# Optimization experiments

Hardware: AMD Instinct MI355X
Metric: run time of the kernel (lower is better)

Reference implementation:

```python
import jax, jax.numpy as jnp
import numpy as np

B, T, N, F_IN, F_OUT, E = 4, 12, 2048, 64, 64, 32768


def setup_inputs() -> dict:
    key = jax.random.key(0)
    ks = jax.random.split(key, 10)
    s = 1.0 / np.sqrt(F_IN)
    return {
        "x": jax.random.normal(ks[0], (B, T, N, F_IN), dtype=jnp.float32),
        "edge_index": jax.random.randint(ks[1], (2, E), 0, N, dtype=jnp.int64),
        "Wk": jax.random.normal(ks[2], (F_IN, F_OUT), dtype=jnp.float32) * s,
        "bk": jax.random.normal(ks[3], (F_OUT,), dtype=jnp.float32) * s,
        "Wq": jax.random.normal(ks[4], (F_IN, F_OUT), dtype=jnp.float32) * s,
        "bq": jax.random.normal(ks[5], (F_OUT,), dtype=jnp.float32) * s,
        "Wv": jax.random.normal(ks[6], (F_IN, F_OUT), dtype=jnp.float32) * s,
        "bv": jax.random.normal(ks[7], (F_OUT,), dtype=jnp.float32) * s,
        "Wskip": jax.random.normal(ks[8], (F_IN, F_OUT), dtype=jnp.float32) * s,
        "bias": jax.random.normal(ks[9], (F_OUT,), dtype=jnp.float32) * s,
    }


def reference(x, edge_index, Wk, bk, Wq, bq, Wv, bv, Wskip, bias):
    b, t, n, _ = x.shape
    xs = x.reshape(b * t, n, -1)                       # (b t) n f
    # per-node projections (small GEMMs)
    k = xs @ Wk + bk                                   # key from target nodes
    q = xs @ Wq + bq                                   # query from source nodes
    v = xs @ Wv + bv                                   # value from source nodes
    src, dst = edge_index[0], edge_index[1]            # j -> i (source_to_target)
    # per-edge gate + message: LeakyReLU(k_i + q_j) * v_j  [(b t), E, f_out]
    msg = jax.nn.leaky_relu(k[:, dst] + q[:, src], negative_slope=0.01) * v[:, src]
    # scatter-add aggregation at target nodes
    agg = jnp.zeros_like(k).at[:, dst].add(msg)
    out = agg + xs @ Wskip + bias
    return out.reshape(b, t, n, -1)
```

## Files before the change

### kernel.cpp

```cpp
#include <hip/hip_runtime.h>

#define BT 48
#define NN 2048
#define FF 64
#define EE 32768
#define ROWS (BT*NN)
#define PRB 256

typedef __attribute__((ext_vector_type(2))) _Float16 half2v;
typedef __attribute__((ext_vector_type(8))) _Float16 half8v;
typedef __attribute__((ext_vector_type(4))) float float4v;

__device__ __forceinline__ unsigned cvt2h(float lo, float hi){
    union { half2v h; unsigned u; } c;
    c.h = half2v{(_Float16)lo, (_Float16)hi};
    return c.u;
}
__device__ __forceinline__ half2v h2(unsigned u){
    union { unsigned u; half2v h; } c; c.u = u; return c.h;
}

__global__ __launch_bounds__(256) void proj_kernel(
    const float* __restrict__ x,
    const float* __restrict__ Wk, const float* __restrict__ bk,
    const float* __restrict__ Wq, const float* __restrict__ bq,
    const float* __restrict__ Wv, const float* __restrict__ bv,
    const float* __restrict__ Ws, const float* __restrict__ bs,
    unsigned* __restrict__ Kh, unsigned* __restrict__ QV,
    float* __restrict__ out, int* __restrict__ meta)
{
    if (blockIdx.x == 0 && threadIdx.x < 8) meta[threadIdx.x] = 0;

    const int tid = threadIdx.x;
    const int w  = tid >> 6;
    const int l  = tid & 63;
    const int lr = l & 15;
    const int lh = l >> 4;
    const float* Wm = (w==0)?Wk:(w==1)?Wq:(w==2)?Wv:Ws;
    const float* bm = (w==0)?bk:(w==1)?bq:(w==2)?bv:bs;

    union FragH { unsigned u[4]; half8v h; };

    FragH af[4][2];
    #pragma unroll
    for (int ft=0;ft<4;ft++)
        #pragma unroll
        for (int h=0;h<2;h++)
            #pragma unroll
            for (int jj=0;jj<4;jj++){
                const int k0 = h*32 + lh*8 + 2*jj;
                af[ft][h].u[jj] = cvt2h(Wm[(size_t)k0*FF + ft*16 + lr],
                                        Wm[(size_t)(k0+1)*FF + ft*16 + lr]);
            }

    float4 bias4[4];
    #pragma unroll
    for (int ft=0;ft<4;ft++) bias4[ft] = *(const float4*)(bm + ft*16 + lh*4);

    const int row0 = blockIdx.x * PRB;
    #pragma unroll 4
    for (int rt=0; rt<PRB/16; ++rt){
        const float* xr = x + (size_t)(row0 + rt*16 + lr)*FF + lh*8;
        const float4 xa0 = *(const float4*)(xr);
        const float4 xa1 = *(const float4*)(xr + 4);
        const float4 xb0 = *(const float4*)(xr + 32);
        const float4 xb1 = *(const float4*)(xr + 36);
        FragH b0, b1;
        b0.u[0]=cvt2h(xa0.x,xa0.y); b0.u[1]=cvt2h(xa0.z,xa0.w);
        b0.u[2]=cvt2h(xa1.x,xa1.y); b0.u[3]=cvt2h(xa1.z,xa1.w);
        b1.u[0]=cvt2h(xb0.x,xb0.y); b1.u[1]=cvt2h(xb0.z,xb0.w);
        b1.u[2]=cvt2h(xb1.x,xb1.y); b1.u[3]=cvt2h(xb1.z,xb1.w);

        const size_t row = (size_t)(row0 + rt*16 + lr);
        #pragma unroll
        for (int ft=0;ft<4;ft++){
            float4v acc = float4v{bias4[ft].x, bias4[ft].y, bias4[ft].z, bias4[ft].w};
            acc = __builtin_amdgcn_mfma_f32_16x16x32_f16(af[ft][0].h, b0.h, acc, 0,0,0);
            acc = __builtin_amdgcn_mfma_f32_16x16x32_f16(af[ft][1].h, b1.h, acc, 0,0,0);
            const int p0 = ft*8 + lh*2;
            if (w == 0){
                uint2 st; st.x = cvt2h(acc[0],acc[1]); st.y = cvt2h(acc[2],acc[3]);
                *(uint2*)(Kh + row*32 + p0) = st;
            } else if (w == 1){
                QV[row*FF + 2*p0]     = cvt2h(acc[0],acc[1]);
                QV[row*FF + 2*(p0+1)] = cvt2h(acc[2],acc[3]);
            } else if (w == 2){
                QV[row*FF + 2*p0 + 1]     = cvt2h(acc[0],acc[1]);
                QV[row*FF + 2*(p0+1) + 1] = cvt2h(acc[2],acc[3]);
            } else {
                *(float4*)(out + row*FF + ft*16 + lh*4) =
                    make_float4(acc[0],acc[1],acc[2],acc[3]);
            }
        }
    }
}

__device__ __forceinline__ void gbar(int* ctr, int nblk){
    __syncthreads();
    if (threadIdx.x == 0){
        __threadfence();
        atomicAdd(ctr, 1);
        while (__hip_atomic_load(ctr, __ATOMIC_ACQUIRE, __HIP_MEMORY_SCOPE_AGENT) < nblk) {}
    }
    __syncthreads();
}

__global__ __launch_bounds__(256) void csr_kernel(
    const unsigned int* __restrict__ ew,
    int* __restrict__ flag, int* __restrict__ bar,
    int* __restrict__ deg, int* __restrict__ offs,
    int* __restrict__ cur, int* __restrict__ elist)
{
    const int t = threadIdx.x, b = blockIdx.x;
    const int gtid = b*256 + t;

    for (int i=gtid; i<NN; i+=16384) deg[i] = 0;
    if (gtid < 16) elist[EE + gtid] = 0;
    unsigned f = 0;
    for (int i=gtid; i<8192; i+=16384) f |= ew[2*i+1];
    if (f) atomicOr((unsigned int*)flag, f);
    gbar(bar+0, 64);
    const bool i64 = (*flag == 0);

    for (int e=gtid; e<EE; e+=16384){
        const int d = i64 ? (int)ew[2*(EE+e)] : (int)ew[EE+e];
        atomicAdd(&deg[d], 1);
    }
    gbar(bar+1, 64);

    if (b == 0){
        __shared__ int wsums[4];
        const int base = t*8;
        int v[8], pre[8];
        #pragma unroll
        for (int j=0;j<8;j++) v[j] = deg[base+j];
        pre[0] = 0;
        #pragma unroll
        for (int j=1;j<8;j++) pre[j] = pre[j-1] + v[j-1];
        const int s = pre[7] + v[7];
        int inc = s;
        const int lane = t & 63, wid = t >> 6;
        #pragma unroll
        for (int d=1; d<64; d<<=1){ int tt = __shfl_up(inc, d, 64); if (lane>=d) inc += tt; }
        if (lane == 63) wsums[wid] = inc;
        __syncthreads();
        if (t == 0){ int a=0; for (int k2=0;k2<4;k2++){ int tt=wsums[k2]; wsums[k2]=a; a+=tt; } }
        __syncthreads();
        const int excl = wsums[wid] + (inc - s);
        #pragma unroll
        for (int j=0;j<8;j++){ offs[base+j] = excl + pre[j]; cur[base+j] = excl + pre[j]; }
        if (t == 255) offs[NN] = excl + s;
    }
    gbar(bar+2, 64);

    for (int e=gtid; e<EE; e+=16384){
        int d, s;
        if (i64){ d = (int)ew[2*(EE+e)]; s = (int)ew[2*e]; }
        else    { d = (int)ew[EE+e];     s = (int)ew[e];   }
        const int pos = atomicAdd(&cur[d], 1);
        elist[pos] = s;
    }
}

#define HEDGE(U) { \
    half2v g01 = k01 + h2((U).x); \
    g01 = __builtin_elementwise_max(g01, g01*c001); \
    acc01 += g01 * h2((U).y); \
    half2v g23 = k23 + h2((U).z); \
    g23 = __builtin_elementwise_max(g23, g23*c001); \
    acc23 += g23 * h2((U).w); }
#define HEDGEM(U, M) { \
    half2v g01 = k01 + h2((U).x); \
    g01 = __builtin_elementwise_max(g01, g01*c001); \
    acc01 += g01 * (h2((U).y) * (M)); \
    half2v g23 = k23 + h2((U).z); \
    g23 = __builtin_elementwise_max(g23, g23*c001); \
    acc23 += g23 * (h2((U).w) * (M)); }

__global__ __launch_bounds__(256) void agg_kernel(
    const unsigned* __restrict__ Kh, const unsigned* __restrict__ QV,
    const int* __restrict__ offs, const int* __restrict__ elist,
    float* __restrict__ out)
{
    const int tid  = threadIdx.x;
    const int lane = tid & 63;
    const int w    = tid >> 6;
    const int b    = blockIdx.x;
    const int xcd  = b & 7;
    const int li   = b >> 3;
    const int bt   = xcd*6 + (li >> 9);
    const int node = ((li & 511) << 2) | w;
    const int sub  = lane >> 4;
    const int fq   = lane & 15;
    const size_t S = (size_t)NN*FF;

    const uint2 ku = *(const uint2*)(Kh + ((size_t)bt*NN + node)*32 + 2*fq);
    const half2v k01 = h2(ku.x), k23 = h2(ku.y);
    const half2v c001 = half2v{(_Float16)0.01f, (_Float16)0.01f};
    const half2v one2 = half2v{(_Float16)1.f, (_Float16)1.f};
    const half2v zero2 = half2v{(_Float16)0.f, (_Float16)0.f};
    const unsigned* QVb = QV + (size_t)bt*S;

    half2v acc01 = zero2, acc23 = zero2;
    const int s0 = offs[node], s1 = offs[node+1];

    for (int i = s0; i < s1; i += 16){
        const int rem  = s1 - i;
        const int4 ev = *(const int4*)(elist + i + 4*sub);
        const uint4 u0 = *(const uint4*)(QVb + (((unsigned)ev.x)<<6) + (fq<<2));
        const uint4 u1 = *(const uint4*)(QVb + (((unsigned)ev.y)<<6) + (fq<<2));
        const uint4 u2 = *(const uint4*)(QVb + (((unsigned)ev.z)<<6) + (fq<<2));
        const uint4 u3 = *(const uint4*)(QVb + (((unsigned)ev.w)<<6) + (fq<<2));
        if (rem >= 16){
            HEDGE(u0); HEDGE(u1); HEDGE(u2); HEDGE(u3);
        } else {
            const half2v m0 = (4*sub+0 < rem) ? one2 : zero2;
            const half2v m1 = (4*sub+1 < rem) ? one2 : zero2;
            const half2v m2 = (4*sub+2 < rem) ? one2 : zero2;
            const half2v m3 = (4*sub+3 < rem) ? one2 : zero2;
            HEDGEM(u0, m0); HEDGEM(u1, m1); HEDGEM(u2, m2); HEDGEM(u3, m3);
        }
    }

    float4 acc = make_float4((float)acc01[0], (float)acc01[1],
                             (float)acc23[0], (float)acc23[1]);

    acc.x += __shfl_xor(acc.x, 16, 64); acc.y += __shfl_xor(acc.y, 16, 64);
    acc.z += __shfl_xor(acc.z, 16, 64); acc.w += __shfl_xor(acc.w, 16, 64);
    acc.x += __shfl_xor(acc.x, 32, 64); acc.y += __shfl_xor(acc.y, 32, 64);
    acc.z += __shfl_xor(acc.z, 32, 64); acc.w += __shfl_xor(acc.w, 32, 64);

    if (sub == 0){
        const size_t rowb = ((size_t)bt*NN + node)*FF;
        const float4 sk = *(const float4*)(out + rowb + fq*4);
        float4 r;
        r.x = acc.x + sk.x; r.y = acc.y + sk.y;
        r.z = acc.z + sk.z; r.w = acc.w + sk.w;
        *(float4*)(out + rowb + fq*4) = r;
    }
}

extern "C" void kernel_launch(void* const* d_in, const int* in_sizes, int n_in,
                              void* d_out, int out_size, void* d_ws, size_t ws_size,
                              hipStream_t stream)
{
    const float* x  = (const float*)d_in[0];
    const unsigned int* ew = (const unsigned int*)d_in[1];
    const float* Wk = (const float*)d_in[2];
    const float* bk = (const float*)d_in[3];
    const float* Wq = (const float*)d_in[4];
    const float* bq = (const float*)d_in[5];
    const float* Wv = (const float*)d_in[6];
    const float* bv = (const float*)d_in[7];
    const float* Ws = (const float*)d_in[8];
    const float* bs = (const float*)d_in[9];
    float* out = (float*)d_out;

    const size_t n = (size_t)ROWS*FF;
    unsigned* Kh = (unsigned*)d_ws;
    unsigned* QV = Kh + (size_t)ROWS*32;
    int* meta  = (int*)(QV + n);
    int* flag  = meta;
    int* bar   = meta + 4;
    int* deg   = meta + 16;
    int* offs  = deg + NN;
    int* cur   = offs + NN + 16;
    int* elist = cur + NN;

    hipLaunchKernelGGL(proj_kernel, dim3(ROWS/PRB), dim3(256), 0, stream,
                       x, Wk,bk, Wq,bq, Wv,bv, Ws,bs, Kh, QV, out, meta);
    hipLaunchKernelGGL(csr_kernel, dim3(64), dim3(256), 0, stream,
                       ew, flag, bar, deg, offs, cur, elist);
    hipLaunchKernelGGL(agg_kernel, dim3(ROWS/4), dim3(256), 0, stream,
                       Kh, QV, offs, elist, out);
}
```

Baseline: 103.5 us.

## Prepack weights, pair projections per wave, and aggregate two timesteps per node

Adds a one-block kernel that converts the four weight matrices once into packed half-precision MFMA fragment layout, so projection blocks load fragments directly instead of converting them per block. The projection kernel now gives each wave two matrices (K+skip or Q+V), which lets Q and V be stored together as one 16-byte write, and uses smaller row tiles across more blocks. The aggregation kernel now handles two batch-timesteps per node in each wave, reusing the edge-list loads and CSR offsets across both and issuing twice as many independent gathers per iteration. This trades an extra kernel launch and higher register pressure for less redundant weight conversion, fewer edge-index reads and more memory-level parallelism.

```diff
diff --git a/kernel.cpp b/kernel.cpp
--- a/kernel.cpp
+++ b/kernel.cpp
@@ -5,7 +5,6 @@
 #define FF 64
 #define EE 32768
 #define ROWS (BT*NN)
-#define PRB 256
 
 typedef __attribute__((ext_vector_type(2))) _Float16 half2v;
 typedef __attribute__((ext_vector_type(8))) _Float16 half8v;
@@ -20,47 +19,67 @@
     union { unsigned u; half2v h; } c; c.u = u; return c.h;
 }
 
+union FragH { unsigned u[4]; half8v h; uint4 u4; };
+
+__global__ __launch_bounds__(256) void wpack_kernel(
+    const float* __restrict__ Wk, const float* __restrict__ Wq,
+    const float* __restrict__ Wv, const float* __restrict__ Ws,
+    unsigned* __restrict__ Wp, int* __restrict__ meta)
+{
+    const int t = threadIdx.x;
+    if (t < 8) meta[t] = 0;
+    for (int idx = t; idx < 8192; idx += 256){
+        const int mat = idx >> 11;
+        const int r   = idx & 2047;
+        const int ft  = r >> 9;
+        const int h   = (r >> 8) & 1;
+        const int l   = (r >> 2) & 63;
+        const int jj  = r & 3;
+        const float* W = (mat==0)?Wk:(mat==1)?Wq:(mat==2)?Wv:Ws;
+        const int k0 = h*32 + (l>>4)*8 + 2*jj;
+        const int c  = ft*16 + (l&15);
+        Wp[idx] = cvt2h(W[(size_t)k0*FF + c], W[(size_t)(k0+1)*FF + c]);
+    }
+}
+
 __global__ __launch_bounds__(256) void proj_kernel(
-    const float* __restrict__ x,
-    const float* __restrict__ Wk, const float* __restrict__ bk,
-    const float* __restrict__ Wq, const float* __restrict__ bq,
-    const float* __restrict__ Wv, const float* __restrict__ bv,
-    const float* __restrict__ Ws, const float* __restrict__ bs,
+    const float* __restrict__ x, const unsigned* __restrict__ Wp,
+    const float* __restrict__ bk, const float* __restrict__ bq,
+    const float* __restrict__ bv, const float* __restrict__ bs,
     unsigned* __restrict__ Kh, unsigned* __restrict__ QV,
-    float* __restrict__ out, int* __restrict__ meta)
-{
-    if (blockIdx.x == 0 && threadIdx.x < 8) meta[threadIdx.x] = 0;
-
+    float* __restrict__ out)
+{
     const int tid = threadIdx.x;
     const int w  = tid >> 6;
     const int l  = tid & 63;
     const int lr = l & 15;
     const int lh = l >> 4;
-    const float* Wm = (w==0)?Wk:(w==1)?Wq:(w==2)?Wv:Ws;
-    const float* bm = (w==0)?bk:(w==1)?bq:(w==2)?bv:bs;
-
-    union FragH { unsigned u[4]; half8v h; };
-
-    FragH af[4][2];
+    const int wm = w & 1;
+    const int matA = wm ? 1 : 0;
+    const int matB = wm ? 2 : 3;
+    const float* bmA = wm ? bq : bk;
+    const float* bmB = wm ? bv : bs;
+
+    FragH afA[4][2], afB[4][2];
     #pragma unroll
     for (int ft=0;ft<4;ft++)
         #pragma unroll
-        for (int h=0;h<2;h++)
-            #pragma unroll
-            for (int jj=0;jj<4;jj++){
-                const int k0 = h*32 + lh*8 + 2*jj;
-                af[ft][h].u[jj] = cvt2h(Wm[(size_t)k0*FF + ft*16 + lr],
-                                        Wm[(size_t)(k0+1)*FF + ft*16 + lr]);
-            }
-
-    float4 bias4[4];
+        for (int h=0;h<2;h++){
+            afA[ft][h].u4 = *(const uint4*)(Wp + ((matA*4+ft)*2+h)*256 + l*4);
+            afB[ft][h].u4 = *(const uint4*)(Wp + ((matB*4+ft)*2+h)*256 + l*4);
+        }
+    float4 biasA[4], biasB[4];
     #pragma unroll
-    for (int ft=0;ft<4;ft++) bias4[ft] = *(const float4*)(bm + ft*16 + lh*4);
-
-    const int row0 = blockIdx.x * PRB;
-    #pragma unroll 4
-    for (int rt=0; rt<PRB/16; ++rt){
-        const float* xr = x + (size_t)(row0 + rt*16 + lr)*FF + lh*8;
+    for (int ft=0;ft<4;ft++){
+        biasA[ft] = *(const float4*)(bmA + ft*16 + lh*4);
+        biasB[ft] = *(const float4*)(bmB + ft*16 + lh*4);
+    }
+
+    const int row0 = blockIdx.x * 128 + (w>>1)*64;
+    #pragma unroll 2
+    for (int rt=0; rt<4; ++rt){
+        const int r16 = row0 + rt*16;
+        const float* xr = x + (size_t)(r16 + lr)*FF + lh*8;
         const float4 xa0 = *(const float4*)(xr);
         const float4 xa1 = *(const float4*)(xr + 4);
         const float4 xb0 = *(const float4*)(xr + 32);
@@ -71,25 +90,25 @@
         b1.u[0]=cvt2h(xb0.x,xb0.y); b1.u[1]=cvt2h(xb0.z,xb0.w);
         b1.u[2]=cvt2h(xb1.x,xb1.y); b1.u[3]=cvt2h(xb1.z,xb1.w);
 
-        const size_t row = (size_t)(row0 + rt*16 + lr);
+        const size_t row = (size_t)(r16 + lr);
         #pragma unroll
         for (int ft=0;ft<4;ft++){
-            float4v acc = float4v{bias4[ft].x, bias4[ft].y, bias4[ft].z, bias4[ft].w};
-            acc = __builtin_amdgcn_mfma_f32_16x16x32_f16(af[ft][0].h, b0.h, acc, 0,0,0);
-            acc = __builtin_amdgcn_mfma_f32_16x16x32_f16(af[ft][1].h, b1.h, acc, 0,0,0);
-            const int p0 = ft*8 + lh*2;
-            if (w == 0){
-                uint2 st; st.x = cvt2h(acc[0],acc[1]); st.y = cvt2h(acc[2],acc[3]);
-                *(uint2*)(Kh + row*32 + p0) = st;
-            } else if (w == 1){
-                QV[row*FF + 2*p0]     = cvt2h(acc[0],acc[1]);
-                QV[row*FF + 2*(p0+1)] = cvt2h(acc[2],acc[3]);
-            } else if (w == 2){
-                QV[row*FF + 2*p0 + 1]     = cvt2h(acc[0],acc[1]);
-                QV[row*FF + 2*(p0+1) + 1] = cvt2h(acc[2],acc[3]);
+            float4v aA = float4v{biasA[ft].x, biasA[ft].y, biasA[ft].z, biasA[ft].w};
+            aA = __builtin_amdgcn_mfma_f32_16x16x32_f16(afA[ft][0].h, b0.h, aA, 0,0,0);
+            aA = __builtin_amdgcn_mfma_f32_16x16x32_f16(afA[ft][1].h, b1.h, aA, 0,0,0);
+            float4v aB = float4v{biasB[ft].x, biasB[ft].y, biasB[ft].z, biasB[ft].w};
+            aB = __builtin_amdgcn_mfma_f32_16x16x32_f16(afB[ft][0].h, b0.h, aB, 0,0,0);
+            aB = __builtin_amdgcn_mfma_f32_16x16x32_f16(afB[ft][1].h, b1.h, aB, 0,0,0);
+            if (wm == 0){
+                uint2 st; st.x = cvt2h(aA[0],aA[1]); st.y = cvt2h(aA[2],aA[3]);
+                *(uint2*)(Kh + row*32 + ft*8 + lh*2) = st;
+                *(float4*)(out + row*FF + ft*16 + lh*4) =
+                    make_float4(aB[0],aB[1],aB[2],aB[3]);
             } else {
-                *(float4*)(out + row*FF + ft*16 + lh*4) =
-                    make_float4(acc[0],acc[1],acc[2],acc[3]);
+                uint4 st;
+                st.x = cvt2h(aA[0],aA[1]); st.y = cvt2h(aB[0],aB[1]);
+                st.z = cvt2h(aA[2],aA[3]); st.w = cvt2h(aB[2],aB[3]);
+                *(uint4*)(QV + row*FF + ft*16 + lh*4) = st;
             }
         }
     }
@@ -162,20 +181,20 @@
     }
 }
 
-#define HEDGE(U) { \
-    half2v g01 = k01 + h2((U).x); \
+#define HEDGE2(U, KA, KB, A01, A23) { \
+    half2v g01 = (KA) + h2((U).x); \
     g01 = __builtin_elementwise_max(g01, g01*c001); \
-    acc01 += g01 * h2((U).y); \
-    half2v g23 = k23 + h2((U).z); \
+    (A01) += g01 * h2((U).y); \
+    half2v g23 = (KB) + h2((U).z); \
     g23 = __builtin_elementwise_max(g23, g23*c001); \
-    acc23 += g23 * h2((U).w); }
-#define HEDGEM(U, M) { \
-    half2v g01 = k01 + h2((U).x); \
+    (A23) += g23 * h2((U).w); }
+#define HEDGE2M(U, KA, KB, A01, A23, M) { \
+    half2v g01 = (KA) + h2((U).x); \
     g01 = __builtin_elementwise_max(g01, g01*c001); \
-    acc01 += g01 * (h2((U).y) * (M)); \
-    half2v g23 = k23 + h2((U).z); \
+    (A01) += g01 * (h2((U).y) * (M)); \
+    half2v g23 = (KB) + h2((U).z); \
     g23 = __builtin_elementwise_max(g23, g23*c001); \
-    acc23 += g23 * (h2((U).w) * (M)); }
+    (A23) += g23 * (h2((U).w) * (M)); }
 
 __global__ __launch_bounds__(256) void agg_kernel(
     const unsigned* __restrict__ Kh, const unsigned* __restrict__ QV,
@@ -188,55 +207,82 @@
     const int b    = blockIdx.x;
     const int xcd  = b & 7;
     const int li   = b >> 3;
-    const int bt   = xcd*6 + (li >> 9);
+    const int pr   = xcd*3 + (li >> 9);
     const int node = ((li & 511) << 2) | w;
     const int sub  = lane >> 4;
     const int fq   = lane & 15;
+    const int bt0  = pr*2;
     const size_t S = (size_t)NN*FF;
 
-    const uint2 ku = *(const uint2*)(Kh + ((size_t)bt*NN + node)*32 + 2*fq);
-    const half2v k01 = h2(ku.x), k23 = h2(ku.y);
+    const uint2 ku0 = *(const uint2*)(Kh + ((size_t)bt0*NN + node)*32 + 2*fq);
+    const uint2 ku1 = *(const uint2*)(Kh + ((size_t)(bt0+1)*NN + node)*32 + 2*fq);
+    const half2v k01a = h2(ku0.x), k23a = h2(ku0.y);
+    const half2v k01b = h2(ku1.x), k23b = h2(ku1.y);
     const half2v c001 = half2v{(_Float16)0.01f, (_Float16)0.01f};
     const half2v one2 = half2v{(_Float16)1.f, (_Float16)1.f};
     const half2v zero2 = half2v{(_Float16)0.f, (_Float16)0.f};
-    const unsigned* QVb = QV + (size_t)bt*S;
-
-    half2v acc01 = zero2, acc23 = zero2;
+    const unsigned* QV0 = QV + (size_t)bt0*S;
+    const unsigned* QV1 = QV0 + S;
+
+    half2v a01_0 = zero2, a23_0 = zero2;
+    half2v a01_1 = zero2, a23_1 = zero2;
     const int s0 = offs[node], s1 = offs[node+1];
 
     for (int i = s0; i < s1; i += 16){
         const int rem  = s1 - i;
         const int4 ev = *(const int4*)(elist + i + 4*sub);
-        const uint4 u0 = *(const uint4*)(QVb + (((unsigned)ev.x)<<6) + (fq<<2));
-        const uint4 u1 = *(const uint4*)(QVb + (((unsigned)ev.y)<<6) + (fq<<2));
-        const uint4 u2 = *(const uint4*)(QVb + (((unsigned)ev.z)<<6) + (fq<<2));
-        const uint4 u3 = *(const uint4*)(QVb + (((unsigned)ev.w)<<6) + (fq<<2));
+        const unsigned o0 = (((unsigned)ev.x)<<6) + (fq<<2);
+        const unsigned o1 = (((unsigned)ev.y)<<6) + (fq<<2);
+        const unsigned o2 = (((unsigned)ev.z)<<6) + (fq<<2);
+        const unsigned o3 = (((unsigned)ev.w)<<6) + (fq<<2);
+        const uint4 u00 = *(const uint4*)(QV0 + o0);
+        const uint4 u10 = *(const uint4*)(QV1 + o0);
+        const uint4 u01 = *(const uint4*)(QV0 + o1);
+        const uint4 u11 = *(const uint4*)(QV1 + o1);
+        const uint4 u02 = *(const uint4*)(QV0 + o2);
+        const uint4 u12 = *(const uint4*)(QV1 + o2);
+        const uint4 u03 = *(const uint4*)(QV0 + o3);
+        const uint4 u13 = *(const uint4*)(QV1 + o3);
         if (rem >= 16){
-            HEDGE(u0); HEDGE(u1); HEDGE(u2); HEDGE(u3);
+            HEDGE2(u00, k01a, k23a, a01_0, a23_0); HEDGE2(u10, k01b, k23b, a01_1, a23_1);
+            HEDGE2(u01, k01a, k23a, a01_0, a23_0); HEDGE2(u11, k01b, k23b, a01_1, a23_1);
+            HEDGE2(u02, k01a, k23a, a01_0, a23_0); HEDGE2(u12, k01b, k23b, a01_1, a23_1);
+            HEDGE2(u03, k01a, k23a, a01_0, a23_0); HEDGE2(u13, k01b, k23b, a01_1, a23_1);
         } else {
             const half2v m0 = (4*sub+0 < rem) ? one2 : zero2;
             const half2v m1 = (4*sub+1 < rem) ? one2 : zero2;
             const half2v m2 = (4*sub+2 < rem) ? one2 : zero2;
             const half2v m3 = (4*sub+3 < rem) ? one2 : zero2;
-            HEDGEM(u0, m0); HEDGEM(u1, m1); HEDGEM(u2, m2); HEDGEM(u3, m3);
+            HEDGE2M(u00, k01a, k23a, a01_0, a23_0, m0); HEDGE2M(u10, k01b, k23b, a01_1, a23_1, m0);
+            HEDGE2M(u01, k01a, k23a, a01_0, a23_0, m1); HEDGE2M(u11, k01b, k23b, a01_1, a23_1, m1);
+            HEDGE2M(u02, k01a, k23a, a01_0, a23_0, m2); HEDGE2M(u12, k01b, k23b, a01_1, a23_1, m2);
+            HEDGE2M(u03, k01a, k23a, a01_0, a23_0, m3); HEDGE2M(u13, k01b, k23b, a01_1, a23_1, m3);
         }
     }
 
-    float4 acc = make_float4((float)acc01[0], (float)acc01[1],
-                             (float)acc23[0], (float)acc23[1]);
-
-    acc.x += __shfl_xor(acc.x, 16, 64); acc.y += __shfl_xor(acc.y, 16, 64);
-    acc.z += __shfl_xor(acc.z, 16, 64); acc.w += __shfl_xor(acc.w, 16, 64);
-    acc.x += __shfl_xor(acc.x, 32, 64); acc.y += __shfl_xor(acc.y, 32, 64);
-    acc.z += __shfl_xor(acc.z, 32, 64); acc.w += __shfl_xor(acc.w, 32, 64);
+    float4 ac0 = make_float4((float)a01_0[0], (float)a01_0[1],
+                             (float)a23_0[0], (float)a23_0[1]);
+    float4 ac1 = make_float4((float)a01_1[0], (float)a01_1[1],
+                             (float)a23_1[0], (float)a23_1[1]);
+
+    ac0.x += __shfl_xor(ac0.x, 16, 64); ac0.y += __shfl_xor(ac0.y, 16, 64);
+    ac0.z += __shfl_xor(ac0.z, 16, 64); ac0.w += __shfl_xor(ac0.w, 16, 64);
+    ac0.x += __shfl_xor(ac0.x, 32, 64); ac0.y += __shfl_xor(ac0.y, 32, 64);
+    ac0.z += __shfl_xor(ac0.z, 32, 64); ac0.w += __shfl_xor(ac0.w, 32, 64);
+    ac1.x += __shfl_xor(ac1.x, 16, 64); ac1.y += __shfl_xor(ac1.y, 16, 64);
+    ac1.z += __shfl_xor(ac1.z, 16, 64); ac1.w += __shfl_xor(ac1.w, 16, 64);
+    ac1.x += __shfl_xor(ac1.x, 32, 64); ac1.y += __shfl_xor(ac1.y, 32, 64);
+    ac1.z += __shfl_xor(ac1.z, 32, 64); ac1.w += __shfl_xor(ac1.w, 32, 64);
 
     if (sub == 0){
-        const size_t rowb = ((size_t)bt*NN + node)*FF;
-        const float4 sk = *(const float4*)(out + rowb + fq*4);
-        float4 r;
-        r.x = acc.x + sk.x; r.y = acc.y + sk.y;
-        r.z = acc.z + sk.z; r.w = acc.w + sk.w;
-        *(float4*)(out + rowb + fq*4) = r;
+        const size_t r0 = ((size_t)bt0*NN + node)*FF;
+        const size_t r1 = r0 + S;
+        const float4 sk0 = *(const float4*)(out + r0 + fq*4);
+        const float4 sk1 = *(const float4*)(out + r1 + fq*4);
+        *(float4*)(out + r0 + fq*4) =
+            make_float4(ac0.x+sk0.x, ac0.y+sk0.y, ac0.z+sk0.z, ac0.w+sk0.w);
+        *(float4*)(out + r1 + fq*4) =
+            make_float4(ac1.x+sk1.x, ac1.y+sk1.y, ac1.z+sk1.z, ac1.w+sk1.w);
     }
 }
 
@@ -259,7 +305,8 @@
     const size_t n = (size_t)ROWS*FF;
     unsigned* Kh = (unsigned*)d_ws;
     unsigned* QV = Kh + (size_t)ROWS*32;
-    int* meta  = (int*)(QV + n);
+    unsigned* Wp = QV + n;
+    int* meta  = (int*)(Wp + 8192);
     int* flag  = meta;
     int* bar   = meta + 4;
     int* deg   = meta + 16;
@@ -267,10 +314,12 @@
     int* cur   = offs + NN + 16;
     int* elist = cur + NN;
 
-    hipLaunchKernelGGL(proj_kernel, dim3(ROWS/PRB), dim3(256), 0, stream,
-                       x, Wk,bk, Wq,bq, Wv,bv, Ws,bs, Kh, QV, out, meta);
+    hipLaunchKernelGGL(wpack_kernel, dim3(1), dim3(256), 0, stream,
+                       Wk, Wq, Wv, Ws, Wp, meta);
+    hipLaunchKernelGGL(proj_kernel, dim3(ROWS/128), dim3(256), 0, stream,
+                       x, Wp, bk, bq, bv, bs, Kh, QV, out);
     hipLaunchKernelGGL(csr_kernel, dim3(64), dim3(256), 0, stream,
                        ew, flag, bar, deg, offs, cur, elist);
-    hipLaunchKernelGGL(agg_kernel, dim3(ROWS/4), dim3(256), 0, stream,
+    hipLaunchKernelGGL(agg_kernel, dim3(ROWS/8), dim3(256), 0, stream,
                        Kh, QV, offs, elist, out);
 }
```

Measured after the change: 95.56 us. 7.7% less time.
